# Optimization experiments

Measured on AMD Instinct MI355X. Metric: run time of the kernel, lower is better.

Reference implementation:

```python
import jax, jax.numpy as jnp
import numpy as np

EPS = 1e-8

def setup_inputs() -> dict:
    key = jax.random.key(0)
    k1, k2 = jax.random.split(key)
    B, D, H, W, K = 32, 256, 64, 64, 64
    X = jax.random.normal(k1, (B, D, H, W), dtype=jnp.float32)
    std1 = 1.0 / float(np.sqrt(K * D))
    codewords = jax.random.uniform(k2, (K, D), dtype=jnp.float32, minval=-std1, maxval=std1)
    return {"X": X, "codewords": codewords}

def reference(X, codewords):
    B, D = X.shape[0], X.shape[1]
    # (B, D, H, W) -> (B, N, D)
    Xf = X.reshape(B, D, -1).transpose(0, 2, 1)
    # pairwise cosine similarity: normalize then matmul -> (B, N, K)
    Xn = Xf / jnp.maximum(jnp.linalg.norm(Xf, axis=-1, keepdims=True), EPS)
    Cn = codewords / jnp.maximum(jnp.linalg.norm(codewords, axis=-1, keepdims=True), EPS)
    L = jnp.einsum('bnd,kd->bnk', Xn, Cn)
    A = jax.nn.softmax(L, axis=2)
    # aggregate: E[b,k,d] = sum_n A[b,n,k] * (Xf[b,n,d] - C[k,d])
    # expressed without materializing the (B,N,K,D) residual tensor:
    E = jnp.einsum('bnk,bnd->bkd', A, Xf) - A.sum(axis=1)[:, :, None] * codewords[None, :, :]
    return E
```

## Files before the change

### kernel.cpp

```cpp
#include <hip/hip_runtime.h>
#include <hip/hip_bf16.h>
#include <math.h>

#define BB 32
#define DD 256
#define NN 4096
#define KK 64
#define EPSV 1e-8f
#define XSTR 264

typedef __attribute__((ext_vector_type(8))) short short8;
typedef __attribute__((ext_vector_type(4))) float f32x4;

__device__ __forceinline__ unsigned int bf16pair(float a, float b) {
    unsigned int ua = __float_as_uint(a);
    unsigned int ub = __float_as_uint(b);
    ua += 0x7fffu + ((ua >> 16) & 1u);
    ub += 0x7fffu + ((ub >> 16) & 1u);
    return (ua >> 16) | (ub & 0xffff0000u);
}
__device__ __forceinline__ unsigned short bf16one(float a) {
    unsigned int ua = __float_as_uint(a);
    ua += 0x7fffu + ((ua >> 16) & 1u);
    return (unsigned short)(ua >> 16);
}

__global__ __launch_bounds__(256, 2) void k_fused(const float* __restrict__ X,
                                                  const float* __restrict__ C,
                                                  float* __restrict__ P,
                                                  float* __restrict__ Sp) {
    __shared__ unsigned short xnd_s[64 * XSTR];
    __shared__ unsigned short xdn_s[DD * 64];
    __shared__ unsigned short at_s[KK * 72];
    __shared__ float red_m[4 * 64];
    __shared__ float red_s[4 * 64];
    __shared__ float rn_s[64];
    float* psum = (float*)at_s;

    int t = threadIdx.x;
    int b = blockIdx.x >> 4, chunk = blockIdx.x & 15;
    int w = t >> 6, lane = t & 63, c = lane & 15, g = lane >> 4;
    int q = t >> 4;
    int n4 = c * 4;

    short8 cnf[8];
    {
        int k = 16 * w + c;
        const float* cp = C + k * DD;
        float4 v0[8], v1[8];
        float ss = 0.f;
#pragma unroll
        for (int ks = 0; ks < 8; ks++) {
            v0[ks] = *(const float4*)(cp + 32 * ks + 8 * g);
            v1[ks] = *(const float4*)(cp + 32 * ks + 8 * g + 4);
            ss = fmaf(v0[ks].x, v0[ks].x, ss); ss = fmaf(v0[ks].y, v0[ks].y, ss);
            ss = fmaf(v0[ks].z, v0[ks].z, ss); ss = fmaf(v0[ks].w, v0[ks].w, ss);
            ss = fmaf(v1[ks].x, v1[ks].x, ss); ss = fmaf(v1[ks].y, v1[ks].y, ss);
            ss = fmaf(v1[ks].z, v1[ks].z, ss); ss = fmaf(v1[ks].w, v1[ks].w, ss);
        }
        ss += __shfl_xor(ss, 16);
        ss += __shfl_xor(ss, 32);
        float r = 1.f / fmaxf(sqrtf(ss), EPSV);
#pragma unroll
        for (int ks = 0; ks < 8; ks++) {
            uint4 u;
            u.x = bf16pair(v0[ks].x * r, v0[ks].y * r);
            u.y = bf16pair(v0[ks].z * r, v0[ks].w * r);
            u.z = bf16pair(v1[ks].x * r, v1[ks].y * r);
            u.w = bf16pair(v1[ks].z * r, v1[ks].w * r);
            cnf[ks] = *(short8*)&u;
        }
    }

    f32x4 eacc[4][4];
#pragma unroll
    for (int dt = 0; dt < 4; dt++)
#pragma unroll
        for (int kt = 0; kt < 4; kt++) eacc[dt][kt] = (f32x4){0.f, 0.f, 0.f, 0.f};
    float s_acc[4] = {0.f, 0.f, 0.f, 0.f};

    for (int p = 0; p < 4; p++) {
        int n0 = chunk * 256 + p * 64;
        __syncthreads();

        {
            f32x4 ssn = (f32x4){0.f, 0.f, 0.f, 0.f};
#pragma unroll
            for (int i = 0; i < 4; i++) {
                int dbase = q * 4 + 64 * i;
                const float* xb = X + ((size_t)b * DD + dbase) * NN + n0 + n4;
                float4 r0 = *(const float4*)(xb);
                float4 r1 = *(const float4*)(xb + NN);
                float4 r2 = *(const float4*)(xb + 2 * NN);
                float4 r3 = *(const float4*)(xb + 3 * NN);
                ssn.x = fmaf(r0.x, r0.x, ssn.x); ssn.x = fmaf(r1.x, r1.x, ssn.x);
                ssn.x = fmaf(r2.x, r2.x, ssn.x); ssn.x = fmaf(r3.x, r3.x, ssn.x);
                ssn.y = fmaf(r0.y, r0.y, ssn.y); ssn.y = fmaf(r1.y, r1.y, ssn.y);
                ssn.y = fmaf(r2.y, r2.y, ssn.y); ssn.y = fmaf(r3.y, r3.y, ssn.y);
                ssn.z = fmaf(r0.z, r0.z, ssn.z); ssn.z = fmaf(r1.z, r1.z, ssn.z);
                ssn.z = fmaf(r2.z, r2.z, ssn.z); ssn.z = fmaf(r3.z, r3.z, ssn.z);
                ssn.w = fmaf(r0.w, r0.w, ssn.w); ssn.w = fmaf(r1.w, r1.w, ssn.w);
                ssn.w = fmaf(r2.w, r2.w, ssn.w); ssn.w = fmaf(r3.w, r3.w, ssn.w);
                const float4 rr[4] = {r0, r1, r2, r3};
#pragma unroll
                for (int j = 0; j < 4; j++) {
                    int d = dbase + j;
                    uint2 u;
                    u.x = bf16pair(rr[j].x, rr[j].y);
                    u.y = bf16pair(rr[j].z, rr[j].w);
                    int off = d * 64 + ((((n4 >> 3) ^ (d & 7)) << 3) | (n4 & 7));
                    *(uint2*)(xdn_s + off) = u;
                }
                {
                    float col0[4] = {r0.x, r1.x, r2.x, r3.x};
                    float col1[4] = {r0.y, r1.y, r2.y, r3.y};
                    float col2[4] = {r0.z, r1.z, r2.z, r3.z};
                    float col3[4] = {r0.w, r1.w, r2.w, r3.w};
                    const float* cols[4] = {col0, col1, col2, col3};
#pragma unroll
                    for (int j = 0; j < 4; j++) {
                        int n = n4 + j;
                        const float* cl = cols[j];
                        uint2 u;
                        u.x = bf16pair(cl[0], cl[1]);
                        u.y = bf16pair(cl[2], cl[3]);
                        int blk = (dbase >> 3) ^ ((n >> 2) & 3);
                        int off = n * XSTR + (blk << 3) + (dbase & 7);
                        *(uint2*)(xnd_s + off) = u;
                    }
                }
            }
            *(f32x4*)(psum + q * 64 + n4) = ssn;
        }
        __syncthreads();

        if (t < 64) {
            float ss = 0.f;
#pragma unroll
            for (int j = 0; j < 16; j++) ss += psum[j * 64 + t];
            rn_s[t] = 1.f / fmaxf(sqrtf(ss), EPSV);
        }

        f32x4 lacc[4];
#pragma unroll
        for (int nt = 0; nt < 4; nt++) lacc[nt] = (f32x4){0.f, 0.f, 0.f, 0.f};
#pragma unroll
        for (int ks = 0; ks < 8; ks++) {
            short8 af = cnf[ks];
#pragma unroll
            for (int nt = 0; nt < 4; nt++) {
                int n = nt * 16 + c;
                short8 bf = *(const short8*)(xnd_s + n * XSTR +
                                             (((4 * ks + g) ^ ((n >> 2) & 3)) << 3));
                lacc[nt] = __builtin_amdgcn_mfma_f32_16x16x32_bf16(af, bf, lacc[nt], 0, 0, 0);
            }
        }

#pragma unroll
        for (int nt = 0; nt < 4; nt++) {
            float m0 = fmaxf(fmaxf(lacc[nt][0], lacc[nt][1]), fmaxf(lacc[nt][2], lacc[nt][3]));
            m0 = fmaxf(m0, __shfl_xor(m0, 16));
            m0 = fmaxf(m0, __shfl_xor(m0, 32));
            if (g == 0) red_m[w * 64 + nt * 16 + c] = m0;
        }
        __syncthreads();

        float lv[4][4];
#pragma unroll
        for (int nt = 0; nt < 4; nt++) {
            int n = nt * 16 + c;
            float rn = rn_s[n];
            float mr = fmaxf(fmaxf(red_m[n], red_m[64 + n]),
                             fmaxf(red_m[128 + n], red_m[192 + n]));
            float m = mr * rn;
            float s = 0.f;
#pragma unroll
            for (int r = 0; r < 4; r++) {
                lv[nt][r] = __expf(lacc[nt][r] * rn - m);
                s += lv[nt][r];
            }
            s += __shfl_xor(s, 16);
            s += __shfl_xor(s, 32);
            if (g == 0) red_s[w * 64 + nt * 16 + c] = s;
        }
        __syncthreads();

#pragma unroll
        for (int nt = 0; nt < 4; nt++) {
            int n = nt * 16 + c;
            float denom = red_s[n] + red_s[64 + n] + red_s[128 + n] + red_s[192 + n];
            float inv = 1.f / denom;
#pragma unroll
            for (int r = 0; r < 4; r++) {
                float a = lv[nt][r] * inv;
                s_acc[r] += a;
                int k = 16 * w + 4 * g + r;
                at_s[k * 72 + ((((n >> 3) ^ (k & 7)) << 3) | (n & 7))] = bf16one(a);
            }
        }
        __syncthreads();

#pragma unroll
        for (int ks2 = 0; ks2 < 2; ks2++) {
            short8 bk[4];
#pragma unroll
            for (int kt = 0; kt < 4; kt++) {
                int k = kt * 16 + c;
                bk[kt] = *(const short8*)(at_s + k * 72 + (((4 * ks2 + g) ^ (k & 7)) << 3));
            }
#pragma unroll
            for (int dt = 0; dt < 4; dt++) {
                int d = w * 64 + dt * 16 + c;
                short8 af = *(const short8*)(xdn_s + d * 64 + (((4 * ks2 + g) ^ (d & 7)) << 3));
#pragma unroll
                for (int kt = 0; kt < 4; kt++)
                    eacc[dt][kt] =
                        __builtin_amdgcn_mfma_f32_16x16x32_bf16(af, bk[kt], eacc[dt][kt], 0, 0, 0);
            }
        }
    }

    float* Pb = P + (size_t)blockIdx.x * (DD * KK);
#pragma unroll
    for (int dt = 0; dt < 4; dt++)
#pragma unroll
        for (int kt = 0; kt < 4; kt++)
#pragma unroll
            for (int r = 0; r < 4; r++) {
                int d = w * 64 + dt * 16 + 4 * g + r;
                Pb[d * 64 + kt * 16 + c] = eacc[dt][kt][r];
            }
#pragma unroll
    for (int r = 0; r < 4; r++) {
        float v = s_acc[r];
        v += __shfl_xor(v, 1);
        v += __shfl_xor(v, 2);
        v += __shfl_xor(v, 4);
        v += __shfl_xor(v, 8);
        if (c == 0) Sp[blockIdx.x * 64 + 16 * w + 4 * g + r] = v;
    }
}

__global__ __launch_bounds__(256) void k_fin(const float* __restrict__ P,
                                             const float* __restrict__ Sp,
                                             const float* __restrict__ C,
                                             float* __restrict__ out) {
    int idx = blockIdx.x * 256 + threadIdx.x;
    int b = idx >> 14;
    int r = idx & 16383;
    int d = r >> 6;
    int k = r & 63;
    float e = 0.f, s = 0.f;
    int base = b * 16;
#pragma unroll
    for (int cc = 0; cc < 16; cc++) {
        e += P[(size_t)(base + cc) * (DD * KK) + d * 64 + k];
        s += Sp[(base + cc) * 64 + k];
    }
    out[(size_t)(b * 64 + k) * 256 + d] = e - s * C[k * 256 + d];
}

extern "C" void kernel_launch(void* const* d_in, const int* in_sizes, int n_in,
                              void* d_out, int out_size, void* d_ws, size_t ws_size,
                              hipStream_t stream) {
    const float* X = (const float*)d_in[0];
    const float* C = (const float*)d_in[1];
    float* out = (float*)d_out;
    unsigned char* ws = (unsigned char*)d_ws;

    float* Sp = (float*)ws;
    float* P = (float*)(ws + 131072);

    k_fused<<<512, 256, 0, stream>>>(X, C, P, Sp);
    k_fin<<<2048, 256, 0, stream>>>(P, Sp, C, out);
}
```

Baseline: 214.7 us.

## Register-prefetch next X tile, drop softmax max pass, shuffle-reduce norms

Loads for the next 64-column X tile are issued into registers before the current tile's compute, so global-load latency overlaps the MFMA and softmax work. Softmax drops the max-subtraction pass and one barrier, relying on cosine logits being bounded in [-1,1]. Per-column norm partials are reduced with wave shuffles and finished by each thread, removing the single-warp serial reduction and its barrier. bf16 packing switches to the HIP intrinsic. The costs are 64 extra VGPRs for the prefetch buffer, which may hurt occupancy under the 2-block launch bound, and softmax is no longer stabilized against large logits.

Result: slower. 234.0 us (+9.0%).

```diff
diff --git a/kernel.cpp b/kernel.cpp
--- a/kernel.cpp
+++ b/kernel.cpp
@@ -13,11 +13,8 @@
 typedef __attribute__((ext_vector_type(4))) float f32x4;
 
 __device__ __forceinline__ unsigned int bf16pair(float a, float b) {
-    unsigned int ua = __float_as_uint(a);
-    unsigned int ub = __float_as_uint(b);
-    ua += 0x7fffu + ((ua >> 16) & 1u);
-    ub += 0x7fffu + ((ub >> 16) & 1u);
-    return (ua >> 16) | (ub & 0xffff0000u);
+    __hip_bfloat162 h = __float22bfloat162_rn(make_float2(a, b));
+    return *(unsigned int*)&h;
 }
 __device__ __forceinline__ unsigned short bf16one(float a) {
     unsigned int ua = __float_as_uint(a);
@@ -32,16 +29,24 @@
     __shared__ unsigned short xnd_s[64 * XSTR];
     __shared__ unsigned short xdn_s[DD * 64];
     __shared__ unsigned short at_s[KK * 72];
-    __shared__ float red_m[4 * 64];
+    __shared__ float rn4[4 * 64];
     __shared__ float red_s[4 * 64];
-    __shared__ float rn_s[64];
-    float* psum = (float*)at_s;
 
     int t = threadIdx.x;
     int b = blockIdx.x >> 4, chunk = blockIdx.x & 15;
     int w = t >> 6, lane = t & 63, c = lane & 15, g = lane >> 4;
     int q = t >> 4;
     int n4 = c * 4;
+
+    const float* Xb = X + (size_t)b * DD * NN + chunk * 256;
+
+    float4 pre[16];
+#pragma unroll
+    for (int i = 0; i < 4; i++) {
+        const float* xb = Xb + (size_t)(q * 4 + 64 * i) * NN + n4;
+#pragma unroll
+        for (int j = 0; j < 4; j++) pre[i * 4 + j] = *(const float4*)(xb + (size_t)j * NN);
+    }
 
     short8 cnf[8];
     {
@@ -80,66 +85,65 @@
     float s_acc[4] = {0.f, 0.f, 0.f, 0.f};
 
     for (int p = 0; p < 4; p++) {
-        int n0 = chunk * 256 + p * 64;
-        __syncthreads();
-
-        {
-            f32x4 ssn = (f32x4){0.f, 0.f, 0.f, 0.f};
+        __syncthreads();
+
+        f32x4 ssn = (f32x4){0.f, 0.f, 0.f, 0.f};
+#pragma unroll
+        for (int i = 0; i < 4; i++) {
+            int dbase = q * 4 + 64 * i;
+            float4 r0 = pre[i * 4 + 0], r1 = pre[i * 4 + 1];
+            float4 r2 = pre[i * 4 + 2], r3 = pre[i * 4 + 3];
+            ssn.x = fmaf(r0.x, r0.x, ssn.x); ssn.x = fmaf(r1.x, r1.x, ssn.x);
+            ssn.x = fmaf(r2.x, r2.x, ssn.x); ssn.x = fmaf(r3.x, r3.x, ssn.x);
+            ssn.y = fmaf(r0.y, r0.y, ssn.y); ssn.y = fmaf(r1.y, r1.y, ssn.y);
+            ssn.y = fmaf(r2.y, r2.y, ssn.y); ssn.y = fmaf(r3.y, r3.y, ssn.y);
+            ssn.z = fmaf(r0.z, r0.z, ssn.z); ssn.z = fmaf(r1.z, r1.z, ssn.z);
+            ssn.z = fmaf(r2.z, r2.z, ssn.z); ssn.z = fmaf(r3.z, r3.z, ssn.z);
+            ssn.w = fmaf(r0.w, r0.w, ssn.w); ssn.w = fmaf(r1.w, r1.w, ssn.w);
+            ssn.w = fmaf(r2.w, r2.w, ssn.w); ssn.w = fmaf(r3.w, r3.w, ssn.w);
+            const float4 rr[4] = {r0, r1, r2, r3};
+#pragma unroll
+            for (int j = 0; j < 4; j++) {
+                int d = dbase + j;
+                uint2 u;
+                u.x = bf16pair(rr[j].x, rr[j].y);
+                u.y = bf16pair(rr[j].z, rr[j].w);
+                int off = d * 64 + ((((n4 >> 3) ^ (d & 7)) << 3) | (n4 & 7));
+                *(uint2*)(xdn_s + off) = u;
+            }
+            {
+                float col[4][4] = {{r0.x, r1.x, r2.x, r3.x},
+                                   {r0.y, r1.y, r2.y, r3.y},
+                                   {r0.z, r1.z, r2.z, r3.z},
+                                   {r0.w, r1.w, r2.w, r3.w}};
+#pragma unroll
+                for (int j = 0; j < 4; j++) {
+                    int n = n4 + j;
+                    uint2 u;
+                    u.x = bf16pair(col[j][0], col[j][1]);
+                    u.y = bf16pair(col[j][2], col[j][3]);
+                    int blk = (dbase >> 3) ^ ((n >> 2) & 3);
+                    *(uint2*)(xnd_s + n * XSTR + (blk << 3) + (dbase & 7)) = u;
+                }
+            }
+        }
+
+        if (p < 3) {
 #pragma unroll
             for (int i = 0; i < 4; i++) {
-                int dbase = q * 4 + 64 * i;
-                const float* xb = X + ((size_t)b * DD + dbase) * NN + n0 + n4;
-                float4 r0 = *(const float4*)(xb);
-                float4 r1 = *(const float4*)(xb + NN);
-                float4 r2 = *(const float4*)(xb + 2 * NN);
-                float4 r3 = *(const float4*)(xb + 3 * NN);
-                ssn.x = fmaf(r0.x, r0.x, ssn.x); ssn.x = fmaf(r1.x, r1.x, ssn.x);
-                ssn.x = fmaf(r2.x, r2.x, ssn.x); ssn.x = fmaf(r3.x, r3.x, ssn.x);
-                ssn.y = fmaf(r0.y, r0.y, ssn.y); ssn.y = fmaf(r1.y, r1.y, ssn.y);
-                ssn.y = fmaf(r2.y, r2.y, ssn.y); ssn.y = fmaf(r3.y, r3.y, ssn.y);
-                ssn.z = fmaf(r0.z, r0.z, ssn.z); ssn.z = fmaf(r1.z, r1.z, ssn.z);
-                ssn.z = fmaf(r2.z, r2.z, ssn.z); ssn.z = fmaf(r3.z, r3.z, ssn.z);
-                ssn.w = fmaf(r0.w, r0.w, ssn.w); ssn.w = fmaf(r1.w, r1.w, ssn.w);
-                ssn.w = fmaf(r2.w, r2.w, ssn.w); ssn.w = fmaf(r3.w, r3.w, ssn.w);
-                const float4 rr[4] = {r0, r1, r2, r3};
-#pragma unroll
-                for (int j = 0; j < 4; j++) {
-                    int d = dbase + j;
-                    uint2 u;
-                    u.x = bf16pair(rr[j].x, rr[j].y);
-                    u.y = bf16pair(rr[j].z, rr[j].w);
-                    int off = d * 64 + ((((n4 >> 3) ^ (d & 7)) << 3) | (n4 & 7));
-                    *(uint2*)(xdn_s + off) = u;
-                }
-                {
-                    float col0[4] = {r0.x, r1.x, r2.x, r3.x};
-                    float col1[4] = {r0.y, r1.y, r2.y, r3.y};
-                    float col2[4] = {r0.z, r1.z, r2.z, r3.z};
-                    float col3[4] = {r0.w, r1.w, r2.w, r3.w};
-                    const float* cols[4] = {col0, col1, col2, col3};
-#pragma unroll
-                    for (int j = 0; j < 4; j++) {
-                        int n = n4 + j;
-                        const float* cl = cols[j];
-                        uint2 u;
-                        u.x = bf16pair(cl[0], cl[1]);
-                        u.y = bf16pair(cl[2], cl[3]);
-                        int blk = (dbase >> 3) ^ ((n >> 2) & 3);
-                        int off = n * XSTR + (blk << 3) + (dbase & 7);
-                        *(uint2*)(xnd_s + off) = u;
-                    }
-                }
-            }
-            *(f32x4*)(psum + q * 64 + n4) = ssn;
-        }
-        __syncthreads();
-
-        if (t < 64) {
-            float ss = 0.f;
-#pragma unroll
-            for (int j = 0; j < 16; j++) ss += psum[j * 64 + t];
-            rn_s[t] = 1.f / fmaxf(sqrtf(ss), EPSV);
-        }
+                const float* xb = Xb + (size_t)(q * 4 + 64 * i) * NN + (p + 1) * 64 + n4;
+#pragma unroll
+                for (int j = 0; j < 4; j++) pre[i * 4 + j] = *(const float4*)(xb + (size_t)j * NN);
+            }
+        }
+
+        ssn.x += __shfl_xor(ssn.x, 16); ssn.x += __shfl_xor(ssn.x, 32);
+        ssn.y += __shfl_xor(ssn.y, 16); ssn.y += __shfl_xor(ssn.y, 32);
+        ssn.z += __shfl_xor(ssn.z, 16); ssn.z += __shfl_xor(ssn.z, 32);
+        ssn.w += __shfl_xor(ssn.w, 16); ssn.w += __shfl_xor(ssn.w, 32);
+        if (g == 0) *(f32x4*)(rn4 + w * 64 + n4) = ssn;
+
+        __syncthreads();
 
         f32x4 lacc[4];
 #pragma unroll
@@ -156,32 +160,21 @@
             }
         }
 
-#pragma unroll
-        for (int nt = 0; nt < 4; nt++) {
-            float m0 = fmaxf(fmaxf(lacc[nt][0], lacc[nt][1]), fmaxf(lacc[nt][2], lacc[nt][3]));
-            m0 = fmaxf(m0, __shfl_xor(m0, 16));
-            m0 = fmaxf(m0, __shfl_xor(m0, 32));
-            if (g == 0) red_m[w * 64 + nt * 16 + c] = m0;
-        }
-        __syncthreads();
-
         float lv[4][4];
 #pragma unroll
         for (int nt = 0; nt < 4; nt++) {
             int n = nt * 16 + c;
-            float rn = rn_s[n];
-            float mr = fmaxf(fmaxf(red_m[n], red_m[64 + n]),
-                             fmaxf(red_m[128 + n], red_m[192 + n]));
-            float m = mr * rn;
+            float ssq = rn4[n] + rn4[64 + n] + rn4[128 + n] + rn4[192 + n];
+            float rn = 1.f / fmaxf(sqrtf(ssq), EPSV);
             float s = 0.f;
 #pragma unroll
             for (int r = 0; r < 4; r++) {
-                lv[nt][r] = __expf(lacc[nt][r] * rn - m);
+                lv[nt][r] = __expf(lacc[nt][r] * rn);
                 s += lv[nt][r];
             }
             s += __shfl_xor(s, 16);
             s += __shfl_xor(s, 32);
-            if (g == 0) red_s[w * 64 + nt * 16 + c] = s;
+            if (g == 0) red_s[w * 64 + n] = s;
         }
         __syncthreads();
 
```
